# Kernel optimization log

Measured on AMD Instinct MI355X. Metric: run time of the kernel, lower is better.

The kernel has to match this reference:

```python
import jax, jax.numpy as jnp
import numpy as np

B, D_IN, H, D, K = 16384, 784, 400, 512, 8192


def setup_inputs() -> dict:
    key = jax.random.key(0)
    ks = jax.random.split(key, 7)
    s = 0.02
    return {
        "x": jax.random.uniform(ks[0], (B, D_IN), dtype=jnp.float32),
        "W1": jax.random.normal(ks[1], (D_IN, H), dtype=jnp.float32) * s,
        "b1": jnp.zeros((H,), jnp.float32),
        "W2": jax.random.normal(ks[2], (H, D), dtype=jnp.float32) * s,
        "b2": jnp.zeros((D,), jnp.float32),
        "W3": jax.random.normal(ks[3], (D, H), dtype=jnp.float32) * s,
        "b3": jnp.zeros((H,), jnp.float32),
        "W4": jax.random.normal(ks[4], (H, D_IN), dtype=jnp.float32) * s,
        "b4": jnp.zeros((D_IN,), jnp.float32),
        "emb": jax.random.normal(ks[5], (K, D), dtype=jnp.float32) * s,
    }


def reference(x, W1, b1, W2, b2, W3, b3, W4, b4, emb):
    batch_size = x.shape[0]
    # encode
    h1 = jax.nn.relu(x @ W1 + b1)
    z_e = h1 @ W2 + b2                               # (B, D)
    # vector quantization: squared L2 dist via expansion (same math as
    # sum((z_e[:,None,:]-emb[None,:,:])**2, -1) without the (B,K,D) temp)
    d = (jnp.sum(z_e * z_e, -1, keepdims=True)
         - 2.0 * (z_e @ emb.T)
         + jnp.sum(emb * emb, -1))                   # (B, K)
    idx = jnp.argmin(d, axis=-1)                     # (B,)
    z_q = emb[idx]                                   # (B, D)
    # decode (torch decodes a detached z_q)
    z_q_dec = jax.lax.stop_gradient(z_q)
    h3 = jax.nn.relu(z_q_dec @ W3 + b3)
    x_reconst = jax.nn.sigmoid(h3 @ W4 + b4)         # (B, 784)
    # BCE, mean reduction (torch F.binary_cross_entropy default)
    p = jnp.clip(x_reconst, 1e-7, 1.0 - 1e-7)
    reconst_loss = -jnp.mean(x * jnp.log(p) + (1.0 - x) * jnp.log1p(-p))
    # codebook loss: grad only to emb (z_e detached)
    embed_loss = jnp.sum((jax.lax.stop_gradient(z_e) - z_q) ** 2) / batch_size
    # commitment loss: grad only to encoder (z_q detached)
    commit_loss = jnp.sum((z_e - jax.lax.stop_gradient(z_q)) ** 2) / batch_size
    return x_reconst, reconst_loss, embed_loss, commit_loss
```

## Files before the change

kernel.cpp:

```cpp
#include <hip/hip_runtime.h>
#include <cfloat>
#include <cstddef>

#define B_SZ 16384
#define DIN  784
#define H_SZ 400
#define D_SZ 512
#define K_SZ 8192

#define DIN_P 800
#define H_P   416

#define ZSCALE 64.f
#define ESCALE 256.f
#define SQSCALE (ZSCALE * ESCALE)

typedef short bf16x8 __attribute__((ext_vector_type(8)));
typedef float f32x4  __attribute__((ext_vector_type(4)));
typedef int   i32x4  __attribute__((ext_vector_type(4)));
typedef int   i32x8  __attribute__((ext_vector_type(8)));

__device__ __forceinline__ unsigned short f2bf(float f) {
  unsigned u = __float_as_uint(f);
  unsigned r = (u + 0x7FFFu + ((u >> 16) & 1u)) >> 16;
  return (unsigned short)r;
}
__device__ __forceinline__ float bf2f(unsigned short h) {
  return __uint_as_float(((unsigned)h) << 16);
}
__device__ __forceinline__ unsigned f2e4m3(float f) {
  unsigned u = __float_as_uint(f);
  const unsigned sign = (u >> 24) & 0x80u;
  const float af = __uint_as_float(u & 0x7FFFFFFFu);
  if (af >= 448.f) return sign | 0x7Eu;
  if (af < 0.015625f) {
    const int m = (int)(af * 512.f + 0.5f);
    return sign | (unsigned)m;
  }
  u = (u & 0x7FFFFFFFu) + 0x7FFFFu + ((u >> 20) & 1u);
  const unsigned e8 = (u >> 23) - 120u;
  if (e8 >= 16u) return sign | 0x7Eu;
  return sign | (e8 << 3) | ((u >> 20) & 7u);
}

__global__ __launch_bounds__(256)
void embprep_kernel(const float* __restrict__ emb,
                    unsigned short* __restrict__ embb,
                    unsigned char* __restrict__ embf,
                    float* __restrict__ esqh, float* __restrict__ accum) {
  if (blockIdx.x == 0 && threadIdx.x == 0) { accum[0] = 0.f; accum[1] = 0.f; }
  const int row  = blockIdx.x * 4 + (threadIdx.x >> 6);
  const int lane = threadIdx.x & 63;
  const float* p = emb + (size_t)row * D_SZ + lane * 8;
  const float4 v0 = *reinterpret_cast<const float4*>(p);
  const float4 v1 = *reinterpret_cast<const float4*>(p + 4);

  ushort4 h0, h1;
  h0.x = f2bf(v0.x); h0.y = f2bf(v0.y); h0.z = f2bf(v0.z); h0.w = f2bf(v0.w);
  h1.x = f2bf(v1.x); h1.y = f2bf(v1.y); h1.z = f2bf(v1.z); h1.w = f2bf(v1.w);
  reinterpret_cast<ushort4*>(embb + (size_t)row * D_SZ + lane * 8)[0] = h0;
  reinterpret_cast<ushort4*>(embb + (size_t)row * D_SZ + lane * 8 + 4)[0] = h1;

  uint2 q;
  q.x = f2e4m3(v0.x * ESCALE) | (f2e4m3(v0.y * ESCALE) << 8) |
        (f2e4m3(v0.z * ESCALE) << 16) | (f2e4m3(v0.w * ESCALE) << 24);
  q.y = f2e4m3(v1.x * ESCALE) | (f2e4m3(v1.y * ESCALE) << 8) |
        (f2e4m3(v1.z * ESCALE) << 16) | (f2e4m3(v1.w * ESCALE) << 24);
  *reinterpret_cast<uint2*>(embf + (size_t)row * D_SZ + lane * 8) = q;

  float s = v0.x * v0.x + v0.y * v0.y + v0.z * v0.z + v0.w * v0.w +
            v1.x * v1.x + v1.y * v1.y + v1.z * v1.z + v1.w * v1.w;
#pragma unroll
  for (int off = 32; off > 0; off >>= 1) s += __shfl_down(s, off);
  if (lane == 0) esqh[row] = 0.5f * SQSCALE * s;
}

__global__ __launch_bounds__(256)
void castpad_x_kernel(const float* __restrict__ x, unsigned short* __restrict__ xb) {
  int u = blockIdx.x * 256 + threadIdx.x;
  const int total = B_SZ * 200;
  const int stride = gridDim.x * 256;
  for (; u < total; u += stride) {
    const int row = u / 200, c4 = u - row * 200;
    ushort4 o = make_ushort4(0, 0, 0, 0);
    if (c4 < 196) {
      float4 v = *reinterpret_cast<const float4*>(x + (size_t)row * DIN + c4 * 4);
      o.x = f2bf(v.x); o.y = f2bf(v.y); o.z = f2bf(v.z); o.w = f2bf(v.w);
    }
    *reinterpret_cast<ushort4*>(xb + (size_t)row * DIN_P + c4 * 4) = o;
  }
}

struct WtransArgs {
  const float* W[4];
  unsigned short* Wt[4];
  int K[4], N[4], Kpad[4], Npad[4], gx[4], off[5];
};

__global__ __launch_bounds__(256)
void wtrans4_kernel(WtransArgs args) {
  __shared__ float t[32][33];
  const int bid = blockIdx.x;
  int i = 0;
#pragma unroll
  for (int j = 1; j < 4; ++j) i += (bid >= args.off[j]);
  const int local = bid - args.off[i];
  const int k0 = (local % args.gx[i]) * 32;
  const int n0 = (local / args.gx[i]) * 32;
  const float* W = args.W[i];
  unsigned short* Wt = args.Wt[i];
  const int K = args.K[i], N = args.N[i];
  const int Kpad = args.Kpad[i], Npad = args.Npad[i];

  const int tx = threadIdx.x & 31, ty = threadIdx.x >> 5;
#pragma unroll
  for (int s = 0; s < 4; ++s) {
    const int k = k0 + ty + s * 8, n = n0 + tx;
    t[ty + s * 8][tx] = (k < K && n < N) ? W[(size_t)k * N + n] : 0.f;
  }
  __syncthreads();
#pragma unroll
  for (int s = 0; s < 4; ++s) {
    const int n = n0 + ty + s * 8, k = k0 + tx;
    if (n < Npad && k < Kpad)
      Wt[(size_t)n * Kpad + k] = f2bf(t[tx][ty + s * 8]);
  }
}

template <int ACT, bool GATHER, bool BCE, bool OUTF32, bool FP8OUT>
__global__ __launch_bounds__(256, 3)
void mgemm_kernel(const unsigned short* __restrict__ A,
                  const unsigned short* __restrict__ Bt,
                  const float* __restrict__ bias, void* __restrict__ C,
                  int N, int Kpad, int NpadOut,
                  const int* __restrict__ gidx,
                  const float* __restrict__ xg, float* __restrict__ loss_accum,
                  unsigned char* __restrict__ C8) {
  __shared__ __align__(16) unsigned short As[2][128 * 32];
  __shared__ __align__(16) unsigned short Bs[2][128 * 32];
  __shared__ int   sidx[128];
  __shared__ float rsum[256];

  const int tid  = threadIdx.x;
  const int w    = tid >> 6, lane = tid & 63;
  const int wr   = w >> 1, wc = w & 1;

  const int nwg = gridDim.x * gridDim.y;
  int bid = blockIdx.y * gridDim.x + blockIdx.x;
  bid = (bid & 7) * (nwg >> 3) + (bid >> 3);
  const int bx = bid % gridDim.x, by = bid / gridDim.x;
  const int rowBase = by * 128, colBase = bx * 128;

  if (GATHER) {
    if (tid < 128) sidx[tid] = gidx[rowBase + tid];
    __syncthreads();
  }

  const int srow  = lane >> 2;
  const int sunit = lane & 3;

  auto stageA = [&](int kt, int bb) {
#pragma unroll
    for (int c = 0; c < 2; ++c) {
      const int rowq = (c * 4 + w) * 16 + srow;
      const long arow = GATHER ? (long)sidx[rowq] : (long)(rowBase + rowq);
      const unsigned short* g = A + (size_t)arow * Kpad + kt * 32 + sunit * 8;
      __builtin_amdgcn_global_load_lds(
          (const __attribute__((address_space(1))) unsigned int*)g,
          (__attribute__((address_space(3))) unsigned int*)
              &As[bb][(((c * 4 + w) * 64) + lane) * 8],
          16, 0, 0);
    }
  };
  auto stageB = [&](int kt, int bb) {
#pragma unroll
    for (int c = 0; c < 2; ++c) {
      const int rowq = (c * 4 + w) * 16 + srow;
      const unsigned short* g =
          Bt + (size_t)(colBase + rowq) * Kpad + kt * 32 + sunit * 8;
      __builtin_amdgcn_global_load_lds(
          (const __attribute__((address_space(1))) unsigned int*)g,
          (__attribute__((address_space(3))) unsigned int*)
              &Bs[bb][(((c * 4 + w) * 64) + lane) * 8],
          16, 0, 0);
    }
  };

  f32x4 acc[4][4] = {};
  stageA(0, 0); stageB(0, 0);
  const int nk = Kpad >> 5;
  const int lr = lane >> 4, lc = lane & 15;

  for (int kt = 0; kt < nk; ++kt) {
    const int bb = kt & 1;
    __syncthreads();
    if (kt + 1 < nk) { stageA(kt + 1, bb ^ 1); stageB(kt + 1, bb ^ 1); }
    bf16x8 a[4], b[4];
#pragma unroll
    for (int f = 0; f < 4; ++f) {
      const int ra = wr * 64 + f * 16 + lc;
      a[f] = *reinterpret_cast<const bf16x8*>(&As[bb][ra * 32 + lr * 8]);
      const int rb = wc * 64 + f * 16 + lc;
      b[f] = *reinterpret_cast<const bf16x8*>(&Bs[bb][rb * 32 + lr * 8]);
    }
#pragma unroll
    for (int i = 0; i < 4; ++i)
#pragma unroll
      for (int j = 0; j < 4; ++j)
        acc[i][j] =
            __builtin_amdgcn_mfma_f32_16x16x32_bf16(a[i], b[j], acc[i][j], 0, 0, 0);
  }

  float bce = 0.f;
#pragma unroll
  for (int j = 0; j < 4; ++j) {
    const int gcol = colBase + wc * 64 + j * 16 + lc;
    const float bj = (gcol < N) ? bias[gcol] : 0.f;
#pragma unroll
    for (int i = 0; i < 4; ++i) {
      const int growb = rowBase + wr * 64 + i * 16 + lr * 4;
#pragma unroll
      for (int r = 0; r < 4; ++r) {
        float v = acc[i][j][r] + bj;
        if (ACT == 1) v = fmaxf(v, 0.f);
        float e2 = 0.f, ov = v;
        if (ACT == 2) {
          e2 = __builtin_amdgcn_exp2f(v * -1.442695041f);
          ov = __builtin_amdgcn_rcpf(1.f + e2);
        }
        const int grow = growb + r;
        if (OUTF32) {
          if (gcol < N) {
            ((float*)C)[(size_t)grow * N + gcol] = ov;
            if (BCE) {
              const float L =
                  0.69314718056f * __builtin_amdgcn_logf(1.f + e2);
              const float xv = xg[(size_t)grow * N + gcol];
              bce += (xv - 1.f) * v - L;
            }
          }
        } else {
          if (gcol < NpadOut) {
            const unsigned short hv = (gcol < N) ? f2bf(ov) : (unsigned short)0;
            ((unsigned short*)C)[(size_t)grow * NpadOut + gcol] = hv;
            if (FP8OUT)
              C8[(size_t)grow * NpadOut + gcol] =
                  (unsigned char)((gcol < N) ? f2e4m3(ov * ZSCALE) : 0u);
          }
        }
      }
    }
  }

  if (BCE) {
    rsum[tid] = bce;
    __syncthreads();
#pragma unroll
    for (int s = 128; s > 0; s >>= 1) {
      if (tid < s) rsum[tid] += rsum[tid + s];
      __syncthreads();
    }
    if (tid == 0) atomicAdd(loss_accum, rsum[0]);
  }
}

__global__ __launch_bounds__(256, 1)
void vq_mfma_kernel(const unsigned char* __restrict__ zef,
                    const unsigned char* __restrict__ embf,
                    const float* __restrict__ esqh,
                    float* __restrict__ cand_val, int* __restrict__ cand_idx) {
  __shared__ __align__(16) unsigned char etile[2][32 * 512];

  const int tid  = threadIdx.x;
  const int w    = tid >> 6, lane = tid & 63;
  const int cq   = lane >> 4, cr = lane & 15;

  const int chunk    = blockIdx.x & 7;
  const int rowblock = blockIdx.x >> 3;
  const int rowBase  = rowblock * 256;
  const int codeBase = chunk * 1024;

  i32x8 a[4][4];
  {
    const unsigned char* z0 =
        zef + (size_t)(rowBase + w * 64 + cr) * D_SZ + cq * 32;
#pragma unroll
    for (int mf = 0; mf < 4; ++mf)
#pragma unroll
      for (int ks = 0; ks < 4; ++ks)
        a[mf][ks] =
            *reinterpret_cast<const i32x8*>(z0 + mf * 16 * D_SZ + ks * 128);
  }

  float minv[4][4];
  int   mini[4][4];
#pragma unroll
  for (int mf = 0; mf < 4; ++mf)
#pragma unroll
    for (int r4 = 0; r4 < 4; ++r4) { minv[mf][r4] = FLT_MAX; mini[mf][r4] = 0; }

  const int srow  = tid >> 5;
  const int sunit = tid & 31;
  const int soff  = (sunit ^ srow) << 4;
  auto stage = [&](int tt, int bb) {
#pragma unroll
    for (int p = 0; p < 4; ++p) {
      const int row = p * 8 + srow;
      const unsigned char* g =
          embf + (size_t)(codeBase + tt * 32 + row) * D_SZ + soff;
      __builtin_amdgcn_global_load_lds(
          (const __attribute__((address_space(1))) unsigned int*)g,
          (__attribute__((address_space(3))) unsigned int*)
              &etile[bb][(p * 8 + w * 2) * 512 + (lane << 4)],
          16, 0, 0);
    }
  };

  stage(0, 0);
  __syncthreads();

  const int swz = cr & 7;
  const char* lds0 = (const char*)etile[0];
  const char* lds1 = (const char*)etile[1];
  const float* esq_c = esqh + codeBase;

  for (int t = 0; t < 32; ++t) {
    const int bb = t & 1;
    if (t + 1 < 32) stage(t + 1, bb ^ 1);
    const char* buf = bb ? lds1 : lds0;
    const int tb = t * 32;

#pragma unroll
    for (int nf = 0; nf < 2; ++nf) {
      const int rb = (nf * 16 + cr) * 512;
      f32x4 acc4[4] = {};
#pragma unroll
      for (int ks = 0; ks < 4; ++ks) {
        const int ub = (ks << 3) + (cq << 1);
        const i32x4 lo =
            *reinterpret_cast<const i32x4*>(buf + rb + ((ub ^ swz) << 4));
        const i32x4 hi =
            *reinterpret_cast<const i32x4*>(buf + rb + (((ub + 1) ^ swz) << 4));
        const i32x8 bv = __builtin_shufflevector(lo, hi, 0, 1, 2, 3, 4, 5, 6, 7);
#pragma unroll
        for (int mf = 0; mf < 4; ++mf)
          acc4[mf] = __builtin_amdgcn_mfma_scale_f32_16x16x128_f8f6f4(
              a[mf][ks], bv, acc4[mf], 0, 0, 0, 0x7F, 0, 0x7F);
      }
      const int cl = tb + nf * 16 + cr;
      const float h = esq_c[cl];
      const int c = codeBase + cl;
#pragma unroll
      for (int mf = 0; mf < 4; ++mf)
#pragma unroll
        for (int r4 = 0; r4 < 4; ++r4) {
          const float s = h - acc4[mf][r4];
          if (s < minv[mf][r4]) { minv[mf][r4] = s; mini[mf][r4] = c; }
        }
    }
    __syncthreads();
  }

#pragma unroll
  for (int mf = 0; mf < 4; ++mf)
#pragma unroll
    for (int r4 = 0; r4 < 4; ++r4) {
      float v = minv[mf][r4];
      int   i = mini[mf][r4];
#pragma unroll
      for (int m = 1; m < 16; m <<= 1) {
        float ov = __shfl_xor(v, m, 64);
        int   oi = __shfl_xor(i, m, 64);
        if (ov < v || (ov == v && oi < i)) { v = ov; i = oi; }
      }
      if (cr == 0) {
        const int row = rowBase + w * 64 + mf * 16 + cq * 4 + r4;
        cand_val[(size_t)chunk * B_SZ + row] = v;
        cand_idx[(size_t)chunk * B_SZ + row] = i;
      }
    }
}

__global__ __launch_bounds__(256)
void vq_finalize_kernel(const float* __restrict__ cv, const int* __restrict__ ci,
                        int* __restrict__ idx) {
  const int r = blockIdx.x * 256 + threadIdx.x;
  float bv = cv[r];
  int   bi = ci[r];
#pragma unroll
  for (int c = 1; c < 8; ++c) {
    const float v = cv[(size_t)c * B_SZ + r];
    const int  i2 = ci[(size_t)c * B_SZ + r];
    if (v < bv || (v == bv && i2 < bi)) { bv = v; bi = i2; }
  }
  idx[r] = bi;
}

__global__ __launch_bounds__(256)
void vqloss_kernel(const unsigned short* __restrict__ zeb,
                   const float* __restrict__ emb,
                   const int* __restrict__ idx, float* __restrict__ accum) {
  __shared__ float rsum[256];
  const int tid = threadIdx.x;
  const size_t stride = (size_t)gridDim.x * 256;
  const size_t total = (size_t)B_SZ * (D_SZ / 8);
  float s = 0.f;
  for (size_t e = (size_t)blockIdx.x * 256 + tid; e < total; e += stride) {
    const size_t b = e >> 6;
    const int   d8 = (int)(e & 63);
    bf16x8 z = *reinterpret_cast<const bf16x8*>(zeb + b * D_SZ + d8 * 8);
    const float* q = emb + (size_t)idx[b] * D_SZ + d8 * 8;
    const float4 q0 = *reinterpret_cast<const float4*>(q);
    const float4 q1 = *reinterpret_cast<const float4*>(q + 4);
    const float qa[8] = {q0.x, q0.y, q0.z, q0.w, q1.x, q1.y, q1.z, q1.w};
#pragma unroll
    for (int j = 0; j < 8; ++j) {
      const float d = bf2f((unsigned short)z[j]) - qa[j];
      s += d * d;
    }
  }
  rsum[tid] = s;
  __syncthreads();
#pragma unroll
  for (int st = 128; st > 0; st >>= 1) {
    if (tid < st) rsum[tid] += rsum[tid + st];
    __syncthreads();
  }
  if (tid == 0) atomicAdd(accum + 1, rsum[0]);
}

__global__ void finalize_kernel(const float* __restrict__ accum,
                                float* __restrict__ out) {
  const float rl = -accum[0] / ((float)B_SZ * (float)DIN);
  const float el = accum[1] / (float)B_SZ;
  out[(size_t)B_SZ * DIN + 0] = rl;
  out[(size_t)B_SZ * DIN + 1] = el;
  out[(size_t)B_SZ * DIN + 2] = el;
}

extern "C" void kernel_launch(void* const* d_in, const int* in_sizes, int n_in,
                              void* d_out, int out_size, void* d_ws,
                              size_t ws_size, hipStream_t stream) {
  const float* x   = (const float*)d_in[0];
  const float* W1  = (const float*)d_in[1];
  const float* b1  = (const float*)d_in[2];
  const float* W2  = (const float*)d_in[3];
  const float* b2  = (const float*)d_in[4];
  const float* W3  = (const float*)d_in[5];
  const float* b3  = (const float*)d_in[6];
  const float* W4  = (const float*)d_in[7];
  const float* b4  = (const float*)d_in[8];
  const float* emb = (const float*)d_in[9];
  float* out = (float*)d_out;

  char* wsb = (char*)d_ws;
  auto alloc = [&](size_t bytes) {
    char* p = wsb;
    wsb += (bytes + 255) & ~(size_t)255;
    return p;
  };
  const size_t xb_bytes  = (size_t)B_SZ * DIN_P * 2;
  const size_t zeb_bytes = (size_t)B_SZ * D_SZ * 2;
  char* regionA = alloc(xb_bytes);
  unsigned short* xb   = (unsigned short*)regionA;
  unsigned short* zeb  = (unsigned short*)regionA;
  unsigned short* embb = (unsigned short*)(regionA + zeb_bytes);
  char* regionB = alloc((size_t)B_SZ * H_P * 2);
  unsigned short* h1b = (unsigned short*)regionB;
  unsigned short* h3b = (unsigned short*)regionB;
  unsigned short* W1t = (unsigned short*)alloc((size_t)512 * DIN_P * 2);
  unsigned short* W2t = (unsigned short*)alloc((size_t)512 * H_P * 2);
  unsigned short* W3t = (unsigned short*)alloc((size_t)512 * D_SZ * 2);
  unsigned short* W4t = (unsigned short*)alloc((size_t)896 * H_P * 2);
  unsigned char* zef  = (unsigned char*)alloc((size_t)B_SZ * D_SZ);
  unsigned char* embf = (unsigned char*)alloc((size_t)K_SZ * D_SZ);
  float* esqh  = (float*)alloc((size_t)K_SZ * 4);
  float* accum = (float*)alloc(64);
  int*   idx   = (int*)alloc((size_t)B_SZ * 4);
  float* cand_val = (float*)alloc((size_t)8 * B_SZ * 4);
  int*   cand_idx = (int*)alloc((size_t)8 * B_SZ * 4);

  castpad_x_kernel<<<2048, 256, 0, stream>>>(x, xb);
  WtransArgs wa;
  wa.W[0] = W1;  wa.Wt[0] = W1t; wa.K[0] = DIN;  wa.N[0] = H_SZ;
  wa.Kpad[0] = DIN_P; wa.Npad[0] = 512; wa.gx[0] = 25;
  wa.W[1] = W2;  wa.Wt[1] = W2t; wa.K[1] = H_SZ; wa.N[1] = D_SZ;
  wa.Kpad[1] = H_P;   wa.Npad[1] = 512; wa.gx[1] = 13;
  wa.W[2] = W3;  wa.Wt[2] = W3t; wa.K[2] = D_SZ; wa.N[2] = H_SZ;
  wa.Kpad[2] = D_SZ;  wa.Npad[2] = 512; wa.gx[2] = 16;
  wa.W[3] = W4;  wa.Wt[3] = W4t; wa.K[3] = H_SZ; wa.N[3] = DIN;
  wa.Kpad[3] = H_P;   wa.Npad[3] = 896; wa.gx[3] = 13;
  wa.off[0] = 0; wa.off[1] = 400; wa.off[2] = 608; wa.off[3] = 864;
  wa.off[4] = 1228;
  wtrans4_kernel<<<1228, 256, 0, stream>>>(wa);
  mgemm_kernel<1, false, false, false, false>
      <<<dim3(4, B_SZ / 128), 256, 0, stream>>>(
      xb, W1t, b1, h1b, H_SZ, DIN_P, H_P, nullptr, nullptr, nullptr, nullptr);
  embprep_kernel<<<K_SZ / 4, 256, 0, stream>>>(emb, embb, embf, esqh, accum);
  mgemm_kernel<0, false, false, false, true>
      <<<dim3(4, B_SZ / 128), 256, 0, stream>>>(
      h1b, W2t, b2, zeb, D_SZ, H_P, D_SZ, nullptr, nullptr, nullptr, zef);
  vq_mfma_kernel<<<512, 256, 0, stream>>>(zef, embf, esqh, cand_val, cand_idx);
  vq_finalize_kernel<<<B_SZ / 256, 256, 0, stream>>>(cand_val, cand_idx, idx);
  vqloss_kernel<<<1024, 256, 0, stream>>>(zeb, emb, idx, accum);
  mgemm_kernel<1, true, false, false, false>
      <<<dim3(4, B_SZ / 128), 256, 0, stream>>>(
      embb, W3t, b3, h3b, H_SZ, D_SZ, H_P, idx, nullptr, nullptr, nullptr);
  mgemm_kernel<2, false, true, true, false>
      <<<dim3(7, B_SZ / 128), 256, 0, stream>>>(
      h3b, W4t, b4, out, DIN, H_P, DIN, nullptr, x, accum, nullptr);
  finalize_kernel<<<1, 1, 0, stream>>>(accum, out);
}
```

Before: 236.5 us.

## Fuse x fp32-to-bf16 cast into first GEMM and merge VQ finalize into loss kernel

Removes the separate castpad kernel: the first encoder GEMM now loads fp32 x directly, converts it to bf16 in registers and stores it to LDS, replacing the async global_load_lds path for A. The VQ candidate reduction (argmin over 8 chunks) is merged into the VQ loss kernel, which now handles 16 rows per block. Together these drop two launches and the write and re-read of the padded bf16 copy of x. The trade-off is that A staging in GEMM1 becomes synchronous register loads with conversion, reading twice as many bytes and possibly hurting latency hiding in the double-buffered loop.

Measured after the change: 232.8 us. About the same (-1.6%).

```diff
diff --git a/kernel.cpp b/kernel.cpp
--- a/kernel.cpp
+++ b/kernel.cpp
@@ -75,22 +75,6 @@
   if (lane == 0) esqh[row] = 0.5f * SQSCALE * s;
 }
 
-__global__ __launch_bounds__(256)
-void castpad_x_kernel(const float* __restrict__ x, unsigned short* __restrict__ xb) {
-  int u = blockIdx.x * 256 + threadIdx.x;
-  const int total = B_SZ * 200;
-  const int stride = gridDim.x * 256;
-  for (; u < total; u += stride) {
-    const int row = u / 200, c4 = u - row * 200;
-    ushort4 o = make_ushort4(0, 0, 0, 0);
-    if (c4 < 196) {
-      float4 v = *reinterpret_cast<const float4*>(x + (size_t)row * DIN + c4 * 4);
-      o.x = f2bf(v.x); o.y = f2bf(v.y); o.z = f2bf(v.z); o.w = f2bf(v.w);
-    }
-    *reinterpret_cast<ushort4*>(xb + (size_t)row * DIN_P + c4 * 4) = o;
-  }
-}
-
 struct WtransArgs {
   const float* W[4];
   unsigned short* Wt[4];
@@ -127,9 +111,10 @@
   }
 }
 
-template <int ACT, bool GATHER, bool BCE, bool OUTF32, bool FP8OUT>
+template <int ACT, bool GATHER, bool BCE, bool OUTF32, bool FP8OUT, bool CVTA>
 __global__ __launch_bounds__(256, 3)
 void mgemm_kernel(const unsigned short* __restrict__ A,
+                  const float* __restrict__ Af,
                   const unsigned short* __restrict__ Bt,
                   const float* __restrict__ bias, void* __restrict__ C,
                   int N, int Kpad, int NpadOut,
@@ -163,13 +148,29 @@
 #pragma unroll
     for (int c = 0; c < 2; ++c) {
       const int rowq = (c * 4 + w) * 16 + srow;
-      const long arow = GATHER ? (long)sidx[rowq] : (long)(rowBase + rowq);
-      const unsigned short* g = A + (size_t)arow * Kpad + kt * 32 + sunit * 8;
-      __builtin_amdgcn_global_load_lds(
-          (const __attribute__((address_space(1))) unsigned int*)g,
-          (__attribute__((address_space(3))) unsigned int*)
-              &As[bb][(((c * 4 + w) * 64) + lane) * 8],
-          16, 0, 0);
+      if (CVTA) {
+        const int grow = rowBase + rowq;
+        const int k0 = kt * 32 + sunit * 8;
+        bf16x8 v8 = {};
+        if (k0 < DIN) {
+          const float* xp = Af + (size_t)grow * DIN + k0;
+          const float4 f0 = *reinterpret_cast<const float4*>(xp);
+          const float4 f1 = *reinterpret_cast<const float4*>(xp + 4);
+          v8[0] = (short)f2bf(f0.x); v8[1] = (short)f2bf(f0.y);
+          v8[2] = (short)f2bf(f0.z); v8[3] = (short)f2bf(f0.w);
+          v8[4] = (short)f2bf(f1.x); v8[5] = (short)f2bf(f1.y);
+          v8[6] = (short)f2bf(f1.z); v8[7] = (short)f2bf(f1.w);
+        }
+        *reinterpret_cast<bf16x8*>(&As[bb][(((c * 4 + w) * 64) + lane) * 8]) = v8;
+      } else {
+        const long arow = GATHER ? (long)sidx[rowq] : (long)(rowBase + rowq);
+        const unsigned short* g = A + (size_t)arow * Kpad + kt * 32 + sunit * 8;
+        __builtin_amdgcn_global_load_lds(
+            (const __attribute__((address_space(1))) unsigned int*)g,
+            (__attribute__((address_space(3))) unsigned int*)
+                &As[bb][(((c * 4 + w) * 64) + lane) * 8],
+            16, 0, 0);
+      }
     }
   };
   auto stageB = [&](int kt, int bb) {
@@ -382,40 +383,45 @@
 }
 
 __global__ __launch_bounds__(256)
-void vq_finalize_kernel(const float* __restrict__ cv, const int* __restrict__ ci,
-                        int* __restrict__ idx) {
-  const int r = blockIdx.x * 256 + threadIdx.x;
-  float bv = cv[r];
-  int   bi = ci[r];
-#pragma unroll
-  for (int c = 1; c < 8; ++c) {
-    const float v = cv[(size_t)c * B_SZ + r];
-    const int  i2 = ci[(size_t)c * B_SZ + r];
-    if (v < bv || (v == bv && i2 < bi)) { bv = v; bi = i2; }
-  }
-  idx[r] = bi;
-}
-
-__global__ __launch_bounds__(256)
 void vqloss_kernel(const unsigned short* __restrict__ zeb,
                    const float* __restrict__ emb,
-                   const int* __restrict__ idx, float* __restrict__ accum) {
+                   const float* __restrict__ cv, const int* __restrict__ ci,
+                   int* __restrict__ idx, float* __restrict__ accum) {
+  __shared__ int   srow_idx[16];
   __shared__ float rsum[256];
   const int tid = threadIdx.x;
-  const size_t stride = (size_t)gridDim.x * 256;
-  const size_t total = (size_t)B_SZ * (D_SZ / 8);
+  const int r0  = blockIdx.x * 16;
+
+  if (tid < 16) {
+    const int r = r0 + tid;
+    float bv = cv[r];
+    int   bi = ci[r];
+#pragma unroll
+    for (int c = 1; c < 8; ++c) {
+      const float v = cv[(size_t)c * B_SZ + r];
+      const int  i2 = ci[(size_t)c * B_SZ + r];
+      if (v < bv || (v == bv && i2 < bi)) { bv = v; bi = i2; }
+    }
+    srow_idx[tid] = bi;
+    idx[r] = bi;
+  }
+  __syncthreads();
+
+  const int lrow = tid >> 4;
+  const int lu   = tid & 15;
+  const unsigned short* z = zeb + (size_t)(r0 + lrow) * D_SZ;
+  const float* q = emb + (size_t)srow_idx[lrow] * D_SZ;
   float s = 0.f;
-  for (size_t e = (size_t)blockIdx.x * 256 + tid; e < total; e += stride) {
-    const size_t b = e >> 6;
-    const int   d8 = (int)(e & 63);
-    bf16x8 z = *reinterpret_cast<const bf16x8*>(zeb + b * D_SZ + d8 * 8);
-    const float* q = emb + (size_t)idx[b] * D_SZ + d8 * 8;
-    const float4 q0 = *reinterpret_cast<const float4*>(q);
-    const float4 q1 = *reinterpret_cast<const float4*>(q + 4);
+#pragma unroll
+  for (int it = 0; it < 4; ++it) {
+    const int d8 = lu + it * 16;
+    bf16x8 zv = *reinterpret_cast<const bf16x8*>(z + d8 * 8);
+    const float4 q0 = *reinterpret_cast<const float4*>(q + d8 * 8);
+    const float4 q1 = *reinterpret_cast<const float4*>(q + d8 * 8 + 4);
     const float qa[8] = {q0.x, q0.y, q0.z, q0.w, q1.x, q1.y, q1.z, q1.w};
 #pragma unroll
     for (int j = 0; j < 8; ++j) {
-      const float d = bf2f((unsigned short)z[j]) - qa[j];
+      const float d = bf2f((unsigned short)zv[j]) - qa[j];
       s += d * d;
     }
   }
@@ -459,12 +465,8 @@
     wsb += (bytes + 255) & ~(size_t)255;
     return p;
   };
-  const size_t xb_bytes  = (size_t)B_SZ * DIN_P * 2;
-  const size_t zeb_bytes = (size_t)B_SZ * D_SZ * 2;
-  char* regionA = alloc(xb_bytes);
-  unsigned short* xb   = (unsigned short*)regionA;
-  unsigned short* zeb  = (unsigned short*)regionA;
-  unsigned short* embb = (unsigned short*)(regionA + zeb_bytes);
+  unsigned short* zeb  = (unsigned short*)alloc((size_t)B_SZ * D_SZ * 2);
+  unsigned short* embb = (unsigned short*)alloc((size_t)K_SZ * D_SZ * 2);
   char* regionB = alloc((size_t)B_SZ * H_P * 2);
   unsigned short* h1b = (unsigned short*)regionB;
   unsigned short* h3b = (unsigned short*)regionB;
@@ -480,7 +482,6 @@
   float* cand_val = (float*)alloc((size_t)8 * B_SZ * 4);
   int*   cand_idx = (int*)alloc((size_t)8 * B_SZ * 4);
 
-  castpad_x_kernel<<<2048, 256, 0, stream>>>(x, xb);
   WtransArgs wa;
   wa.W[0] = W1;  wa.Wt[0] = W1t; wa.K[0] = DIN;  wa.N[0] = H_SZ;
   wa.Kpad[0] = DIN_P; wa.Npad[0] = 512; wa.gx[0] = 25;
@@ -493,21 +494,24 @@
   wa.off[0] = 0; wa.off[1] = 400; wa.off[2] = 608; wa.off[3] = 864;
   wa.off[4] = 1228;
   wtrans4_kernel<<<1228, 256, 0, stream>>>(wa);
-  mgemm_kernel<1, false, false, false, false>
+  mgemm_kernel<1, false, false, false, false, true>
       <<<dim3(4, B_SZ / 128), 256, 0, stream>>>(
-      xb, W1t, b1, h1b, H_SZ, DIN_P, H_P, nullptr, nullptr, nullptr, nullptr);
+      nullptr, x, W1t, b1, h1b, H_SZ, DIN_P, H_P, nullptr, nullptr, nullptr,
+      nullptr);
   embprep_kernel<<<K_SZ / 4, 256, 0, stream>>>(emb, embb, embf, esqh, accum);
-  mgemm_kernel<0, false, false, false, true>
+  mgemm_kernel<0, false, false, false, true, false>
       <<<dim3(4, B_SZ / 128), 256, 0, stream>>>(
-      h1b, W2t, b2, zeb, D_SZ, H_P, D_SZ, nullptr, nullptr, nullptr, zef);
+      h1b, nullptr, W2t, b2, zeb, D_SZ, H_P, D_SZ, nullptr, nullptr, nullptr,
+      zef);
   vq_mfma_kernel<<<512, 256, 0, stream>>>(zef, embf, esqh, cand_val, cand_idx);
-  vq_finalize_kernel<<<B_SZ / 256, 256, 0, stream>>>(cand_val, cand_idx, idx);
-  vqloss_kernel<<<1024, 256, 0, stream>>>(zeb, emb, idx, accum);
-  mgemm_kernel<1, true, false, false, false>
+  vqloss_kernel<<<B_SZ / 16, 256, 0, stream>>>(zeb, emb, cand_val, cand_idx,
+                                               idx, accum);
+  mgemm_kernel<1, true, false, false, false, false>
       <<<dim3(4, B_SZ / 128), 256, 0, stream>>>(
-      embb, W3t, b3, h3b, H_SZ, D_SZ, H_P, idx, nullptr, nullptr, nullptr);
-  mgemm_kernel<2, false, true, true, false>
+      embb, nullptr, W3t, b3, h3b, H_SZ, D_SZ, H_P, idx, nullptr, nullptr,
+      nullptr);
+  mgemm_kernel<2, false, true, true, false, false>
       <<<dim3(7, B_SZ / 128), 256, 0, stream>>>(
-      h3b, W4t, b4, out, DIN, H_P, DIN, nullptr, x, accum, nullptr);
+      h3b, nullptr, W4t, b4, out, DIN, H_P, DIN, nullptr, x, accum, nullptr);
   finalize_kernel<<<1, 1, 0, stream>>>(accum, out);
 }
```
